# Kernel optimization log

Hardware: AMD Instinct MI355X
Metric: run time of the kernel (lower is better)

## Reference

```python
import jax, jax.numpy as jnp
import numpy as np

N_HEADS = 8
D_EMBED = 512
D_HEAD = D_EMBED // N_HEADS  # used only for the scale factor, as in the source


def setup_inputs() -> dict:
    key = jax.random.key(0)
    k1, k2, k3, k4, k5 = jax.random.split(key, 5)
    B, S, D = 4, 4096, D_EMBED
    s = 1.0 / np.sqrt(D)
    return {
        "x": jax.random.normal(k1, (B, S, D), dtype=jnp.float32),
        "w_in": jax.random.normal(k2, (3 * D, D), dtype=jnp.float32) * s,
        "b_in": jax.random.normal(k3, (3 * D,), dtype=jnp.float32) * 0.01,
        "w_out": jax.random.normal(k4, (D, D), dtype=jnp.float32) * s,
        "b_out": jax.random.normal(k5, (D,), dtype=jnp.float32) * 0.01,
    }


def reference(x, w_in, b_in, w_out, b_out):
    # in_proj: torch Linear y = x @ W.T + b ; chunk into q,k,v along last dim
    qkv = jnp.einsum("bsd,ed->bse", x, w_in) + b_in  # [B,S,3D]
    q, k, v = jnp.split(qkv, 3, axis=-1)  # each [B,S,D]
    # NOTE: source never splits into heads; attention over full d_embed,
    # but scaled by sqrt(d_head) = sqrt(d_embed / n_heads).
    scores = jnp.einsum("bqd,bkd->bqk", q, k) / np.sqrt(D_HEAD)  # [B,S,S]
    weight = jax.nn.softmax(scores, axis=-1)
    out = jnp.einsum("bqk,bkd->bqd", weight, v)  # [B,S,D]
    out = jnp.einsum("bsd,ed->bse", out, w_out) + b_out
    return out
```

## Files before the change

kernel.cpp:

```cpp
#include <hip/hip_runtime.h>

typedef __bf16 bf16x8 __attribute__((ext_vector_type(8)));
typedef float f32x4 __attribute__((ext_vector_type(4)));

#define MFMA16(a, b, c) __builtin_amdgcn_mfma_f32_16x16x32_bf16(a, b, c, 0, 0, 0)
#define LOG2E 1.44269504088896340736f

__device__ __forceinline__ unsigned short f2bf(float f) {
  union { float f; unsigned u; } v; v.f = f;
  return (unsigned short)((v.u + 0x7fffu + ((v.u >> 16) & 1u)) >> 16);
}
__device__ __forceinline__ bf16x8 ld_frag(const unsigned short* p) {
  return *(const bf16x8*)p;
}
__device__ __forceinline__ void gld_lds16(const unsigned short* g, unsigned short* l) {
  __builtin_amdgcn_global_load_lds(
      (const __attribute__((address_space(1))) unsigned int*)(const void*)g,
      (__attribute__((address_space(3))) unsigned int*)(void*)l, 16, 0, 0);
}

__global__ void cvt_f2bf(const float* __restrict__ in,
                         unsigned short* __restrict__ out, int n4) {
  int i = blockIdx.x * blockDim.x + threadIdx.x;
  if (i < n4) {
    float4 v = ((const float4*)in)[i];
    ushort4 o;
    o.x = f2bf(v.x); o.y = f2bf(v.y); o.z = f2bf(v.z); o.w = f2bf(v.w);
    ((ushort4*)out)[i] = o;
  }
}

__global__ void gemm_bt(const unsigned short* __restrict__ A,
                        const unsigned short* __restrict__ B,
                        const float* __restrict__ bias,
                        float* __restrict__ outf,
                        unsigned short* __restrict__ qbuf,
                        unsigned short* __restrict__ kbuf,
                        unsigned short* __restrict__ vtbuf,
                        int M, int N, int K, int mode) {
  __shared__ alignas(16) unsigned short As[128 * 32];
  __shared__ alignas(16) unsigned short Bs[128 * 32];
  const int n0 = blockIdx.x * 128, m0 = blockIdx.y * 128;
  const int tid = threadIdx.x;
  const int l = tid & 63, w = tid >> 6;
  const int quad = l >> 4, c = l & 15;
  const int wm = (w >> 1) * 64, wn = (w & 1) * 64;

  f32x4 acc[4][4] = {};
  const int kiters = K >> 5;
  for (int kt = 0; kt < kiters; ++kt) {
    __syncthreads();
    const int kk = kt * 32 + (l & 3) * 8;
    const int row = l >> 2;
#pragma unroll
    for (int i = 0; i < 2; ++i) {
      const int rbase = i * 64 + w * 16;
      gld_lds16(&A[(size_t)(m0 + rbase + row) * K + kk], &As[rbase * 32]);
      gld_lds16(&B[(size_t)(n0 + rbase + row) * K + kk], &Bs[rbase * 32]);
    }
    __syncthreads();
    bf16x8 af[4], bfr[4];
#pragma unroll
    for (int t = 0; t < 4; ++t) {
      af[t] = ld_frag(&As[(wm + t * 16 + c) * 32 + quad * 8]);
      bfr[t] = ld_frag(&Bs[(wn + t * 16 + c) * 32 + quad * 8]);
    }
#pragma unroll
    for (int mt = 0; mt < 4; ++mt)
#pragma unroll
      for (int nt = 0; nt < 4; ++nt)
        acc[mt][nt] = MFMA16(af[mt], bfr[nt], acc[mt][nt]);
  }

#pragma unroll
  for (int nt = 0; nt < 4; ++nt) {
    const int n = n0 + wn + nt * 16 + c;
    const float bsum = bias[n];
#pragma unroll
    for (int mt = 0; mt < 4; ++mt) {
      const int mbase = m0 + wm + mt * 16 + quad * 4;
      if (mode == 0) {
#pragma unroll
        for (int r = 0; r < 4; ++r)
          outf[(size_t)(mbase + r) * N + n] = acc[mt][nt][r] + bsum;
      } else if (n < 1024) {
        unsigned short* dst = (n < 512) ? qbuf : kbuf;
        const int nn = n & 511;
#pragma unroll
        for (int r = 0; r < 4; ++r)
          dst[(size_t)(mbase + r) * 512 + nn] = f2bf(acc[mt][nt][r] + bsum);
      } else {
        const int d = n - 1024;
        const int bb = mbase >> 12, s = mbase & 4095;
        ushort4 pk;
        pk.x = f2bf(acc[mt][nt][0] + bsum);
        pk.y = f2bf(acc[mt][nt][1] + bsum);
        pk.z = f2bf(acc[mt][nt][2] + bsum);
        pk.w = f2bf(acc[mt][nt][3] + bsum);
        *(ushort4*)&vtbuf[((size_t)bb * 512 + d) * 4096 + s] = pk;
      }
    }
  }
}

#define KROW 520
#define PROW 40
#define KBUF (32 * KROW)

__global__ __launch_bounds__(256, 2) void attn_kernel(
    const unsigned short* __restrict__ Q, const unsigned short* __restrict__ Kb,
    const unsigned short* __restrict__ Vt, unsigned short* __restrict__ part0,
    unsigned short* __restrict__ part1, float2* __restrict__ mlbuf) {
  __shared__ alignas(16) unsigned short k_lds[2 * KBUF];
  __shared__ alignas(16) unsigned short p_lds[64 * PROW];
  __shared__ float alpha_s[64];
  __shared__ int flag_s[4];

  const int bid = blockIdx.x;
  const int xcd = bid & 7;
  const int b = xcd >> 1;
  const int half = (bid >> 3) & 1;
  const int qt = (bid >> 4) | ((xcd & 1) << 5);
  const int s0 = qt * 64;
  const int kvbase = half * 2048;
  const int tid = threadIdx.x;
  const int l = tid & 63, w = tid >> 6;
  const int quad = l >> 4, c = l & 15;
  const size_t boff = (size_t)b * 4096 * 512;

  const unsigned short* Kbase = Kb + boff;

  auto stage_k = [&](int kv0, int bufbase) {
#pragma unroll
    for (int i = 0; i < 8; ++i) {
      const int row = i * 4 + w;
      gld_lds16(&Kbase[(size_t)(kv0 + row) * 512 + l * 8],
                &k_lds[bufbase + row * KROW]);
    }
  };

  stage_k(kvbase, 0);

  bf16x8 qf[16];
  {
    const unsigned short* qrow = Q + boff + (size_t)(s0 + w * 16 + c) * 512;
#pragma unroll
    for (int ks = 0; ks < 16; ++ks) qf[ks] = ld_frag(&qrow[ks * 32 + quad * 8]);
  }

  f32x4 o[8][4] = {};
  float m_run = -1e30f, l_run = 0.f;

  const unsigned short* vrow = Vt + (size_t)b * 512 * 4096 +
                               (size_t)(w * 128 + c) * 4096 + kvbase + quad * 8;

  for (int it = 0; it < 64; ++it) {
    const int cb = (it & 1) * KBUF;

    asm volatile("s_waitcnt vmcnt(0)" ::: "memory");
    __builtin_amdgcn_s_barrier();
    __builtin_amdgcn_sched_barrier(0);

    if (it + 1 < 64) stage_k(kvbase + (it + 1) * 32, KBUF - cb);

    f32x4 sa[2][2] = {};
    __builtin_amdgcn_s_setprio(1);
#pragma unroll
    for (int ks = 0; ks < 16; ++ks) {
      const unsigned short* kr = &k_lds[cb + c * KROW + ks * 32 + quad * 8];
      bf16x8 kf0 = ld_frag(kr);
      bf16x8 kf1 = ld_frag(kr + 16 * KROW);
      sa[0][ks & 1] = MFMA16(kf0, qf[ks], sa[0][ks & 1]);
      sa[1][ks & 1] = MFMA16(kf1, qf[ks], sa[1][ks & 1]);
    }
    __builtin_amdgcn_s_setprio(0);
    const f32x4 s0v = sa[0][0] + sa[0][1];
    const f32x4 s1v = sa[1][0] + sa[1][1];

    const float C1 = 0.125f * LOG2E;
    float m8 = fmaxf(fmaxf(fmaxf(s0v[0], s0v[1]), fmaxf(s0v[2], s0v[3])),
                     fmaxf(fmaxf(s1v[0], s1v[1]), fmaxf(s1v[2], s1v[3])));
    m8 = fmaxf(m8, __shfl_xor(m8, 16));
    m8 = fmaxf(m8, __shfl_xor(m8, 32));

    const bool need = __any(m8 - m_run > 8.0f);
    float alpha = 1.0f;
    if (need) {
      const float mn = fmaxf(m_run, m8);
      alpha = exp2f((m_run - mn) * C1);
      m_run = mn;
      l_run *= alpha;
    }

    float p0[4], p1[4], s8 = 0.f;
#pragma unroll
    for (int r = 0; r < 4; ++r) {
      p0[r] = exp2f((s0v[r] - m_run) * C1);
      p1[r] = exp2f((s1v[r] - m_run) * C1);
      s8 += p0[r] + p1[r];
    }
    unsigned short* prow = &p_lds[(w * 16 + c) * PROW];
    ushort4 pk0, pk1;
    pk0.x = f2bf(p0[0]); pk0.y = f2bf(p0[1]); pk0.z = f2bf(p0[2]); pk0.w = f2bf(p0[3]);
    pk1.x = f2bf(p1[0]); pk1.y = f2bf(p1[1]); pk1.z = f2bf(p1[2]); pk1.w = f2bf(p1[3]);
    *(ushort4*)&prow[quad * 4] = pk0;
    *(ushort4*)&prow[16 + quad * 4] = pk1;

    s8 += __shfl_xor(s8, 16);
    s8 += __shfl_xor(s8, 32);
    l_run += s8;

    if (quad == 0) alpha_s[w * 16 + c] = alpha;
    if (l == 0) flag_s[w] = need ? 1 : 0;

    asm volatile("s_waitcnt lgkmcnt(0)" ::: "memory");
    __builtin_amdgcn_sched_barrier(0);
    __builtin_amdgcn_s_barrier();
    __builtin_amdgcn_sched_barrier(0);

    const int f0 = flag_s[0], f1 = flag_s[1], f2 = flag_s[2], f3 = flag_s[3];
    if (f0) {
      const float a = alpha_s[c];
#pragma unroll
      for (int t = 0; t < 8; ++t) o[t][0] *= a;
    }
    if (f1) {
      const float a = alpha_s[16 + c];
#pragma unroll
      for (int t = 0; t < 8; ++t) o[t][1] *= a;
    }
    if (f2) {
      const float a = alpha_s[32 + c];
#pragma unroll
      for (int t = 0; t < 8; ++t) o[t][2] *= a;
    }
    if (f3) {
      const float a = alpha_s[48 + c];
#pragma unroll
      for (int t = 0; t < 8; ++t) o[t][3] *= a;
    }

    const bf16x8 pf0 = ld_frag(&p_lds[(size_t)c * PROW + quad * 8]);
    const bf16x8 pf1 = ld_frag(&p_lds[(size_t)(16 + c) * PROW + quad * 8]);
    const bf16x8 pf2 = ld_frag(&p_lds[(size_t)(32 + c) * PROW + quad * 8]);
    const bf16x8 pf3 = ld_frag(&p_lds[(size_t)(48 + c) * PROW + quad * 8]);
    const unsigned short* vi = vrow + it * 32;
    __builtin_amdgcn_s_setprio(1);
#pragma unroll
    for (int t = 0; t < 8; ++t) {
      const bf16x8 vf = ld_frag(vi + (size_t)t * 16 * 4096);
      o[t][0] = MFMA16(vf, pf0, o[t][0]);
      o[t][1] = MFMA16(vf, pf1, o[t][1]);
      o[t][2] = MFMA16(vf, pf2, o[t][2]);
      o[t][3] = MFMA16(vf, pf3, o[t][3]);
    }
    __builtin_amdgcn_s_setprio(0);
  }

  __syncthreads();
  if (quad == 0) {
    alpha_s[w * 16 + c] = l_run;
    float2 ml; ml.x = m_run; ml.y = l_run;
    mlbuf[(size_t)half * 16384 + b * 4096 + s0 + w * 16 + c] = ml;
  }
  __syncthreads();
  const float linv0 = 1.0f / alpha_s[c];
  const float linv1 = 1.0f / alpha_s[16 + c];
  const float linv2 = 1.0f / alpha_s[32 + c];
  const float linv3 = 1.0f / alpha_s[48 + c];

  unsigned short* part = half ? part1 : part0;
  unsigned short* obase = part + boff + (size_t)s0 * 512 + w * 128 + quad * 4;
#pragma unroll
  for (int t = 0; t < 8; ++t) {
    const float li[4] = {linv0, linv1, linv2, linv3};
#pragma unroll
    for (int j = 0; j < 4; ++j) {
      ushort4 pk;
      pk.x = f2bf(o[t][j][0] * li[j]);
      pk.y = f2bf(o[t][j][1] * li[j]);
      pk.z = f2bf(o[t][j][2] * li[j]);
      pk.w = f2bf(o[t][j][3] * li[j]);
      *(ushort4*)&obase[(size_t)(j * 16 + c) * 512 + t * 16] = pk;
    }
  }
}

__global__ void merge_halves(const unsigned short* __restrict__ p1,
                             const float2* __restrict__ mlbuf,
                             unsigned short* __restrict__ p0out) {
  const int i = blockIdx.x * blockDim.x + threadIdx.x;
  const int row = i >> 6;
  const float2 a = mlbuf[row];
  const float2 bb = mlbuf[16384 + row];
  const float C1 = 0.125f * LOG2E;
  const float M = fmaxf(a.x, bb.x);
  float w0 = a.y * exp2f((a.x - M) * C1);
  float w1 = bb.y * exp2f((bb.x - M) * C1);
  const float inv = 1.0f / (w0 + w1);
  w0 *= inv; w1 *= inv;
  bf16x8 v0 = *(const bf16x8*)(p0out + (size_t)i * 8);
  bf16x8 v1 = *(const bf16x8*)(p1 + (size_t)i * 8);
  ushort4 o0, o1;
  o0.x = f2bf(w0 * (float)v0[0] + w1 * (float)v1[0]);
  o0.y = f2bf(w0 * (float)v0[1] + w1 * (float)v1[1]);
  o0.z = f2bf(w0 * (float)v0[2] + w1 * (float)v1[2]);
  o0.w = f2bf(w0 * (float)v0[3] + w1 * (float)v1[3]);
  o1.x = f2bf(w0 * (float)v0[4] + w1 * (float)v1[4]);
  o1.y = f2bf(w0 * (float)v0[5] + w1 * (float)v1[5]);
  o1.z = f2bf(w0 * (float)v0[6] + w1 * (float)v1[6]);
  o1.w = f2bf(w0 * (float)v0[7] + w1 * (float)v1[7]);
  *(ushort4*)(p0out + (size_t)i * 8) = o0;
  *(ushort4*)(p0out + (size_t)i * 8 + 4) = o1;
}

extern "C" void kernel_launch(void* const* d_in, const int* in_sizes, int n_in,
                              void* d_out, int out_size, void* d_ws, size_t ws_size,
                              hipStream_t stream) {
  const float* x = (const float*)d_in[0];
  const float* w_in = (const float*)d_in[1];
  const float* b_in = (const float*)d_in[2];
  const float* w_out = (const float*)d_in[3];
  const float* b_out = (const float*)d_in[4];
  float* out = (float*)d_out;

  const size_t MTOT = (size_t)4 * 4096 * 512;
  unsigned short* q = (unsigned short*)d_ws;
  unsigned short* k = q + MTOT;
  unsigned short* vt = k + MTOT;
  unsigned short* xbf = vt + MTOT;
  unsigned short* part1 = xbf + MTOT;
  unsigned short* w_in_bf = part1 + MTOT;
  unsigned short* w_out_bf = w_in_bf + 1536 * 512;
  float2* mlbuf = (float2*)(w_out_bf + 512 * 512);

  cvt_f2bf<<<dim3((int)(MTOT / 4 / 256)), 256, 0, stream>>>(x, xbf,
                                                            (int)(MTOT / 4));
  cvt_f2bf<<<dim3(768), 256, 0, stream>>>(w_in, w_in_bf, 1536 * 512 / 4);
  cvt_f2bf<<<dim3(256), 256, 0, stream>>>(w_out, w_out_bf, 512 * 512 / 4);

  gemm_bt<<<dim3(12, 128), 256, 0, stream>>>(xbf, w_in_bf, b_in, nullptr, q, k,
                                             vt, 16384, 1536, 512, 1);
  attn_kernel<<<dim3(512), 256, 0, stream>>>(q, k, vt, xbf, part1, mlbuf);
  merge_halves<<<dim3(4096), 256, 0, stream>>>(part1, mlbuf, xbf);
  gemm_bt<<<dim3(4, 128), 256, 0, stream>>>(xbf, w_out_bf, b_out, out, nullptr,
                                            nullptr, nullptr, 16384, 512, 512,
                                            0);
}
```

Baseline: 456.3 us.

## Warp-specialize attention into QK/softmax and PV waves with staged V in LDS

The attention kernel now runs 512 threads split into two warp groups. Four waves compute QK^T and softmax for tile it and write P, alpha and flags into double-buffered LDS, while the other four waves stage V tiles into a swizzled LDS buffer and do the PV MFMAs for tile it-1, so the two phases overlap. V is no longer read directly from global memory per fragment. The GEMM also remaps workgroup IDs so consecutive blocks land on the same XCD. In exchange, LDS use and waves per CU go up, and with launch_bounds(512,2) fewer registers are available per thread, which may limit occupancy or cause spills.

```diff
diff --git a/kernel.cpp b/kernel.cpp
--- a/kernel.cpp
+++ b/kernel.cpp
@@ -40,7 +40,12 @@
                         int M, int N, int K, int mode) {
   __shared__ alignas(16) unsigned short As[128 * 32];
   __shared__ alignas(16) unsigned short Bs[128 * 32];
-  const int n0 = blockIdx.x * 128, m0 = blockIdx.y * 128;
+  const int orig = blockIdx.x + gridDim.x * blockIdx.y;
+  const int nx = gridDim.x;
+  const int nwg = nx * gridDim.y;
+  int lid = orig;
+  if ((nwg & 7) == 0) lid = (orig & 7) * (nwg >> 3) + (orig >> 3);
+  const int n0 = (lid % nx) * 128, m0 = (lid / nx) * 128;
   const int tid = threadIdx.x;
   const int l = tid & 63, w = tid >> 6;
   const int quad = l >> 4, c = l & 15;
@@ -105,16 +110,20 @@
 
 #define KROW 520
 #define PROW 40
-#define KBUF (32 * KROW)
-
-__global__ __launch_bounds__(256, 2) void attn_kernel(
+#define KHALF (32 * KROW)
+#define VHALF (512 * 32)
+#define PHALF (64 * PROW)
+
+__global__ __launch_bounds__(512, 2) void attn_kernel(
     const unsigned short* __restrict__ Q, const unsigned short* __restrict__ Kb,
     const unsigned short* __restrict__ Vt, unsigned short* __restrict__ part0,
     unsigned short* __restrict__ part1, float2* __restrict__ mlbuf) {
-  __shared__ alignas(16) unsigned short k_lds[2 * KBUF];
-  __shared__ alignas(16) unsigned short p_lds[64 * PROW];
-  __shared__ float alpha_s[64];
-  __shared__ int flag_s[4];
+  __shared__ alignas(16) unsigned short k_lds[2 * KHALF];
+  __shared__ alignas(16) unsigned short v_lds[2 * VHALF];
+  __shared__ alignas(16) unsigned short p_lds[2 * PHALF];
+  __shared__ float alpha_s[2][64];
+  __shared__ int flag_s[2][4];
+  __shared__ float l_s[64];
 
   const int bid = blockIdx.x;
   const int xcd = bid & 7;
@@ -125,25 +134,39 @@
   const int kvbase = half * 2048;
   const int tid = threadIdx.x;
   const int l = tid & 63, w = tid >> 6;
+  const int wq = w & 3;
+  const bool is_qk = (w < 4);
   const int quad = l >> 4, c = l & 15;
   const size_t boff = (size_t)b * 4096 * 512;
 
   const unsigned short* Kbase = Kb + boff;
-
-  auto stage_k = [&](int kv0, int bufbase) {
+  const unsigned short* Vbase = Vt + (size_t)b * 512 * 4096;
+
+  auto stage_k = [&](int kv0, int bsel) {
 #pragma unroll
     for (int i = 0; i < 8; ++i) {
-      const int row = i * 4 + w;
+      const int row = i * 4 + wq;
       gld_lds16(&Kbase[(size_t)(kv0 + row) * 512 + l * 8],
-                &k_lds[bufbase + row * KROW]);
+                &k_lds[bsel * KHALF + row * KROW]);
     }
   };
-
-  stage_k(kvbase, 0);
+  auto stage_v = [&](int kv0, int bsel) {
+#pragma unroll
+    for (int i = 0; i < 8; ++i) {
+      const int dbase = (i * 4 + wq) * 16;
+      const int d = dbase + (l >> 2);
+      const int jl = (l & 3) ^ ((d >> 1) & 3);
+      gld_lds16(&Vbase[(size_t)d * 4096 + kv0 + jl * 8],
+                &v_lds[bsel * VHALF + dbase * 32]);
+    }
+  };
+
+  if (is_qk) stage_k(kvbase, 0);
+  else       stage_v(kvbase, 0);
 
   bf16x8 qf[16];
-  {
-    const unsigned short* qrow = Q + boff + (size_t)(s0 + w * 16 + c) * 512;
+  if (is_qk) {
+    const unsigned short* qrow = Q + boff + (size_t)(s0 + wq * 16 + c) * 512;
 #pragma unroll
     for (int ks = 0; ks < 16; ++ks) qf[ks] = ld_frag(&qrow[ks * 32 + quad * 8]);
   }
@@ -151,137 +174,158 @@
   f32x4 o[8][4] = {};
   float m_run = -1e30f, l_run = 0.f;
 
-  const unsigned short* vrow = Vt + (size_t)b * 512 * 4096 +
-                               (size_t)(w * 128 + c) * 4096 + kvbase + quad * 8;
-
-  for (int it = 0; it < 64; ++it) {
-    const int cb = (it & 1) * KBUF;
-
-    asm volatile("s_waitcnt vmcnt(0)" ::: "memory");
-    __builtin_amdgcn_s_barrier();
-    __builtin_amdgcn_sched_barrier(0);
-
-    if (it + 1 < 64) stage_k(kvbase + (it + 1) * 32, KBUF - cb);
-
-    f32x4 sa[2][2] = {};
-    __builtin_amdgcn_s_setprio(1);
-#pragma unroll
-    for (int ks = 0; ks < 16; ++ks) {
-      const unsigned short* kr = &k_lds[cb + c * KROW + ks * 32 + quad * 8];
-      bf16x8 kf0 = ld_frag(kr);
-      bf16x8 kf1 = ld_frag(kr + 16 * KROW);
-      sa[0][ks & 1] = MFMA16(kf0, qf[ks], sa[0][ks & 1]);
-      sa[1][ks & 1] = MFMA16(kf1, qf[ks], sa[1][ks & 1]);
-    }
-    __builtin_amdgcn_s_setprio(0);
-    const f32x4 s0v = sa[0][0] + sa[0][1];
-    const f32x4 s1v = sa[1][0] + sa[1][1];
-
-    const float C1 = 0.125f * LOG2E;
-    float m8 = fmaxf(fmaxf(fmaxf(s0v[0], s0v[1]), fmaxf(s0v[2], s0v[3])),
-                     fmaxf(fmaxf(s1v[0], s1v[1]), fmaxf(s1v[2], s1v[3])));
-    m8 = fmaxf(m8, __shfl_xor(m8, 16));
-    m8 = fmaxf(m8, __shfl_xor(m8, 32));
-
-    const bool need = __any(m8 - m_run > 8.0f);
-    float alpha = 1.0f;
-    if (need) {
-      const float mn = fmaxf(m_run, m8);
-      alpha = exp2f((m_run - mn) * C1);
-      m_run = mn;
-      l_run *= alpha;
-    }
-
-    float p0[4], p1[4], s8 = 0.f;
-#pragma unroll
-    for (int r = 0; r < 4; ++r) {
-      p0[r] = exp2f((s0v[r] - m_run) * C1);
-      p1[r] = exp2f((s1v[r] - m_run) * C1);
-      s8 += p0[r] + p1[r];
-    }
-    unsigned short* prow = &p_lds[(w * 16 + c) * PROW];
-    ushort4 pk0, pk1;
-    pk0.x = f2bf(p0[0]); pk0.y = f2bf(p0[1]); pk0.z = f2bf(p0[2]); pk0.w = f2bf(p0[3]);
-    pk1.x = f2bf(p1[0]); pk1.y = f2bf(p1[1]); pk1.z = f2bf(p1[2]); pk1.w = f2bf(p1[3]);
-    *(ushort4*)&prow[quad * 4] = pk0;
-    *(ushort4*)&prow[16 + quad * 4] = pk1;
-
-    s8 += __shfl_xor(s8, 16);
-    s8 += __shfl_xor(s8, 32);
-    l_run += s8;
-
-    if (quad == 0) alpha_s[w * 16 + c] = alpha;
-    if (l == 0) flag_s[w] = need ? 1 : 0;
-
-    asm volatile("s_waitcnt lgkmcnt(0)" ::: "memory");
+  const float C1 = 0.125f * LOG2E;
+  const int jp8 = (quad ^ ((c >> 1) & 3)) * 8;
+
+  for (int it = 0; it <= 64; ++it) {
+    if (is_qk) {
+      if (it < 64) { asm volatile("s_waitcnt vmcnt(0)" ::: "memory"); }
+    } else {
+      if (it >= 1) { asm volatile("s_waitcnt vmcnt(0)" ::: "memory"); }
+    }
     __builtin_amdgcn_sched_barrier(0);
     __builtin_amdgcn_s_barrier();
     __builtin_amdgcn_sched_barrier(0);
 
-    const int f0 = flag_s[0], f1 = flag_s[1], f2 = flag_s[2], f3 = flag_s[3];
-    if (f0) {
-      const float a = alpha_s[c];
-#pragma unroll
-      for (int t = 0; t < 8; ++t) o[t][0] *= a;
-    }
-    if (f1) {
-      const float a = alpha_s[16 + c];
-#pragma unroll
-      for (int t = 0; t < 8; ++t) o[t][1] *= a;
-    }
-    if (f2) {
-      const float a = alpha_s[32 + c];
-#pragma unroll
-      for (int t = 0; t < 8; ++t) o[t][2] *= a;
-    }
-    if (f3) {
-      const float a = alpha_s[48 + c];
-#pragma unroll
-      for (int t = 0; t < 8; ++t) o[t][3] *= a;
-    }
-
-    const bf16x8 pf0 = ld_frag(&p_lds[(size_t)c * PROW + quad * 8]);
-    const bf16x8 pf1 = ld_frag(&p_lds[(size_t)(16 + c) * PROW + quad * 8]);
-    const bf16x8 pf2 = ld_frag(&p_lds[(size_t)(32 + c) * PROW + quad * 8]);
-    const bf16x8 pf3 = ld_frag(&p_lds[(size_t)(48 + c) * PROW + quad * 8]);
-    const unsigned short* vi = vrow + it * 32;
-    __builtin_amdgcn_s_setprio(1);
+    if (is_qk) {
+      if (it < 64) {
+        if (it + 1 < 64) stage_k(kvbase + (it + 1) * 32, (it + 1) & 1);
+
+        const unsigned short* kb2 = &k_lds[(it & 1) * KHALF];
+        f32x4 sa[2][2] = {};
+        __builtin_amdgcn_s_setprio(1);
+#pragma unroll
+        for (int ks = 0; ks < 16; ++ks) {
+          const unsigned short* kr = &kb2[c * KROW + ks * 32 + quad * 8];
+          bf16x8 kf0 = ld_frag(kr);
+          bf16x8 kf1 = ld_frag(kr + 16 * KROW);
+          sa[0][ks & 1] = MFMA16(kf0, qf[ks], sa[0][ks & 1]);
+          sa[1][ks & 1] = MFMA16(kf1, qf[ks], sa[1][ks & 1]);
+        }
+        __builtin_amdgcn_s_setprio(0);
+        const f32x4 s0v = sa[0][0] + sa[0][1];
+        const f32x4 s1v = sa[1][0] + sa[1][1];
+
+        float m8 = fmaxf(fmaxf(fmaxf(s0v[0], s0v[1]), fmaxf(s0v[2], s0v[3])),
+                         fmaxf(fmaxf(s1v[0], s1v[1]), fmaxf(s1v[2], s1v[3])));
+        m8 = fmaxf(m8, __shfl_xor(m8, 16));
+        m8 = fmaxf(m8, __shfl_xor(m8, 32));
+
+        const bool need = __any(m8 - m_run > 8.0f);
+        float alpha = 1.0f;
+        if (need) {
+          const float mn = fmaxf(m_run, m8);
+          alpha = exp2f((m_run - mn) * C1);
+          m_run = mn;
+          l_run *= alpha;
+        }
+
+        float p0[4], p1[4], s8 = 0.f;
+#pragma unroll
+        for (int r = 0; r < 4; ++r) {
+          p0[r] = exp2f((s0v[r] - m_run) * C1);
+          p1[r] = exp2f((s1v[r] - m_run) * C1);
+          s8 += p0[r] + p1[r];
+        }
+        unsigned short* prow =
+            &p_lds[(it & 1) * PHALF + (wq * 16 + c) * PROW];
+        ushort4 pk0, pk1;
+        pk0.x = f2bf(p0[0]); pk0.y = f2bf(p0[1]);
+        pk0.z = f2bf(p0[2]); pk0.w = f2bf(p0[3]);
+        pk1.x = f2bf(p1[0]); pk1.y = f2bf(p1[1]);
+        pk1.z = f2bf(p1[2]); pk1.w = f2bf(p1[3]);
+        *(ushort4*)&prow[quad * 4] = pk0;
+        *(ushort4*)&prow[16 + quad * 4] = pk1;
+
+        s8 += __shfl_xor(s8, 16);
+        s8 += __shfl_xor(s8, 32);
+        l_run += s8;
+
+        if (quad == 0) alpha_s[it & 1][wq * 16 + c] = alpha;
+        if (l == 0) flag_s[it & 1][wq] = need ? 1 : 0;
+
+        asm volatile("s_waitcnt lgkmcnt(0)" ::: "memory");
+        __builtin_amdgcn_sched_barrier(0);
+      }
+    } else {
+      if (it >= 1) {
+        const int pv = it - 1;
+        const int pb = pv & 1;
+        if (it < 64) stage_v(kvbase + it * 32, it & 1);
+
+        const int f0 = flag_s[pb][0], f1 = flag_s[pb][1];
+        const int f2 = flag_s[pb][2], f3 = flag_s[pb][3];
+        if (f0) {
+          const float a = alpha_s[pb][c];
+#pragma unroll
+          for (int t = 0; t < 8; ++t) o[t][0] *= a;
+        }
+        if (f1) {
+          const float a = alpha_s[pb][16 + c];
+#pragma unroll
+          for (int t = 0; t < 8; ++t) o[t][1] *= a;
+        }
+        if (f2) {
+          const float a = alpha_s[pb][32 + c];
+#pragma unroll
+          for (int t = 0; t < 8; ++t) o[t][2] *= a;
+        }
+        if (f3) {
+          const float a = alpha_s[pb][48 + c];
+#pragma unroll
+          for (int t = 0; t < 8; ++t) o[t][3] *= a;
+        }
+
+        const unsigned short* pbb = &p_lds[pb * PHALF];
+        const bf16x8 pf0 = ld_frag(&pbb[(size_t)c * PROW + quad * 8]);
+        const bf16x8 pf1 = ld_frag(&pbb[(size_t)(16 + c) * PROW + quad * 8]);
+        const bf16x8 pf2 = ld_frag(&pbb[(size_t)(32 + c) * PROW + quad * 8]);
+        const bf16x8 pf3 = ld_frag(&pbb[(size_t)(48 + c) * PROW + quad * 8]);
+        const unsigned short* vb = &v_lds[pb * VHALF];
+        __builtin_amdgcn_s_setprio(1);
+#pragma unroll
+        for (int t = 0; t < 8; ++t) {
+          const bf16x8 vf = ld_frag(&vb[(wq * 128 + t * 16 + c) * 32 + jp8]);
+          o[t][0] = MFMA16(vf, pf0, o[t][0]);
+          o[t][1] = MFMA16(vf, pf1, o[t][1]);
+          o[t][2] = MFMA16(vf, pf2, o[t][2]);
+          o[t][3] = MFMA16(vf, pf3, o[t][3]);
+        }
+        __builtin_amdgcn_s_setprio(0);
+
+        asm volatile("s_waitcnt lgkmcnt(0)" ::: "memory");
+        __builtin_amdgcn_sched_barrier(0);
+      }
+    }
+  }
+
+  __syncthreads();
+  if (is_qk && quad == 0) {
+    l_s[wq * 16 + c] = l_run;
+    float2 ml; ml.x = m_run; ml.y = l_run;
+    mlbuf[(size_t)half * 16384 + b * 4096 + s0 + wq * 16 + c] = ml;
+  }
+  __syncthreads();
+  if (!is_qk) {
+    const float linv0 = 1.0f / l_s[c];
+    const float linv1 = 1.0f / l_s[16 + c];
+    const float linv2 = 1.0f / l_s[32 + c];
+    const float linv3 = 1.0f / l_s[48 + c];
+    unsigned short* part = half ? part1 : part0;
+    unsigned short* obase =
+        part + boff + (size_t)s0 * 512 + wq * 128 + quad * 4;
 #pragma unroll
     for (int t = 0; t < 8; ++t) {
-      const bf16x8 vf = ld_frag(vi + (size_t)t * 16 * 4096);
-      o[t][0] = MFMA16(vf, pf0, o[t][0]);
-      o[t][1] = MFMA16(vf, pf1, o[t][1]);
-      o[t][2] = MFMA16(vf, pf2, o[t][2]);
-      o[t][3] = MFMA16(vf, pf3, o[t][3]);
-    }
-    __builtin_amdgcn_s_setprio(0);
-  }
-
-  __syncthreads();
-  if (quad == 0) {
-    alpha_s[w * 16 + c] = l_run;
-    float2 ml; ml.x = m_run; ml.y = l_run;
-    mlbuf[(size_t)half * 16384 + b * 4096 + s0 + w * 16 + c] = ml;
-  }
-  __syncthreads();
-  const float linv0 = 1.0f / alpha_s[c];
-  const float linv1 = 1.0f / alpha_s[16 + c];
-  const float linv2 = 1.0f / alpha_s[32 + c];
-  const float linv3 = 1.0f / alpha_s[48 + c];
-
-  unsigned short* part = half ? part1 : part0;
-  unsigned short* obase = part + boff + (size_t)s0 * 512 + w * 128 + quad * 4;
-#pragma unroll
-  for (int t = 0; t < 8; ++t) {
-    const float li[4] = {linv0, linv1, linv2, linv3};
-#pragma unroll
-    for (int j = 0; j < 4; ++j) {
-      ushort4 pk;
-      pk.x = f2bf(o[t][j][0] * li[j]);
-      pk.y = f2bf(o[t][j][1] * li[j]);
-      pk.z = f2bf(o[t][j][2] * li[j]);
-      pk.w = f2bf(o[t][j][3] * li[j]);
-      *(ushort4*)&obase[(size_t)(j * 16 + c) * 512 + t * 16] = pk;
+      const float li[4] = {linv0, linv1, linv2, linv3};
+#pragma unroll
+      for (int j = 0; j < 4; ++j) {
+        ushort4 pk;
+        pk.x = f2bf(o[t][j][0] * li[j]);
+        pk.y = f2bf(o[t][j][1] * li[j]);
+        pk.z = f2bf(o[t][j][2] * li[j]);
+        pk.w = f2bf(o[t][j][3] * li[j]);
+        *(ushort4*)&obase[(size_t)(j * 16 + c) * 512 + t * 16] = pk;
+      }
     }
   }
 }
@@ -341,7 +385,7 @@
 
   gemm_bt<<<dim3(12, 128), 256, 0, stream>>>(xbf, w_in_bf, b_in, nullptr, q, k,
                                              vt, 16384, 1536, 512, 1);
-  attn_kernel<<<dim3(512), 256, 0, stream>>>(q, k, vt, xbf, part1, mlbuf);
+  attn_kernel<<<dim3(512), 512, 0, stream>>>(q, k, vt, xbf, part1, mlbuf);
   merge_halves<<<dim3(4096), 256, 0, stream>>>(part1, mlbuf, xbf);
   gemm_bt<<<dim3(4, 128), 256, 0, stream>>>(xbf, w_out_bf, b_out, out, nullptr,
                                             nullptr, nullptr, 16384, 512, 512,
```

New measurement: 529.6 us. +16.1%, slower.
